# Performance work log

Hardware: AMD Instinct MI355X
Metric: run time of the kernel (lower is better)

## Reference

```python
import jax, jax.numpy as jnp
import numpy as np

B = 16384
N_DENSE = 13
N_TABLES = 26
VOCAB = 100000
DIM = 64
BOTTOM_DIMS = [13, 512, 256, 64]
TOP_DIMS = [442, 512, 256, 1]
TOP_SIGMOID_POS = 2  # sigmoid on last top layer; bottom uses relu everywhere


def _init_mlp(key, dims, scale=0.05):
    ws, bs = [], []
    for i in range(len(dims) - 1):
        key, k = jax.random.split(key)
        ws.append(jax.random.normal(k, (dims[i], dims[i + 1]), dtype=jnp.float32) * scale)
        bs.append(jnp.zeros((dims[i + 1],), dtype=jnp.float32))
    return ws, bs


def setup_inputs() -> dict:
    key = jax.random.key(0)
    k_dense, k_sparse, k_tab, k_b, k_t = jax.random.split(key, 5)
    dense_inputs = jax.random.normal(k_dense, (B, N_DENSE), dtype=jnp.float32)
    sparse_inputs = jax.random.randint(k_sparse, (B, N_TABLES), 0, VOCAB, dtype=jnp.int64)
    tables = jax.random.normal(k_tab, (N_TABLES, VOCAB, DIM), dtype=jnp.float32) * 0.01
    bws, bbs = _init_mlp(k_b, BOTTOM_DIMS)
    tws, tbs = _init_mlp(k_t, TOP_DIMS)
    return {
        'dense_inputs': dense_inputs, 'sparse_inputs': sparse_inputs, 'tables': tables,
        'bw1': bws[0], 'bb1': bbs[0], 'bw2': bws[1], 'bb2': bbs[1], 'bw3': bws[2], 'bb3': bbs[2],
        'tw1': tws[0], 'tb1': tbs[0], 'tw2': tws[1], 'tb2': tbs[1], 'tw3': tws[2], 'tb3': tbs[2],
    }


def _mlp(x, ws, bs, sigmoid_pos):
    for i, (w, b) in enumerate(zip(ws, bs)):
        x = x @ w + b
        x = jax.nn.sigmoid(x) if (sigmoid_pos is not None and i == sigmoid_pos) else jax.nn.relu(x)
    return x


def reference(dense_inputs, sparse_inputs, tables,
              bw1, bb1, bw2, bb2, bw3, bb3,
              tw1, tb1, tw2, tb2, tw3, tb3):
    # Bottom MLP: [B,13] -> [B,64], relu on every layer
    dx = _mlp(dense_inputs, [bw1, bw2, bw3], [bb1, bb2, bb3], None)
    # Multi-table embedding gather: [B,26] -> [B,26,64]
    sx = tables[jnp.arange(N_TABLES)[None, :], sparse_inputs]
    # Dot interaction (self_interaction=True): stack dense + sparse fields
    T = jnp.concatenate([dx[:, None, :], sx], axis=1)          # [B, 27, 64]
    Z = jnp.einsum('bfd,bgd->bfg', T, T)                        # [B, 27, 27]
    F = N_TABLES + 1
    iu, ju = jnp.triu_indices(F, k=0)                           # include diagonal
    flat = Z[:, iu, ju]                                         # [B, 378]
    interaction = jnp.concatenate([dx, flat], axis=1)           # [B, 442]
    # Top MLP with sigmoid on the last layer
    return _mlp(interaction, [tw1, tw2, tw3], [tb1, tb2, tb3], TOP_SIGMOID_POS)
```

## Files before the change

kernel.cpp:

```cpp
#include <hip/hip_runtime.h>

typedef unsigned short u16;
typedef _Float16 f16;
typedef __attribute__((ext_vector_type(8))) _Float16 half8;
typedef __attribute__((ext_vector_type(4))) float f32x4;
typedef __attribute__((ext_vector_type(16))) float f32x16;

#define DEV __device__ __forceinline__

static constexpr int BATCH   = 16384;
static constexpr int NTAB    = 26;
static constexpr int VOCAB   = 100000;
static constexpr int DIM     = 64;

DEV u16 f2h(float f){ union { f16 h; u16 u; } x; x.h = (f16)f; return x.u; }

DEV void llds16(u16* dst, const u16* src){
  __builtin_amdgcn_global_load_lds(
      (const __attribute__((address_space(1))) unsigned*)src,
      (__attribute__((address_space(3))) unsigned*)dst, 16, 0, 0);
}

DEV int crow(int reg, int half){ return (reg & 3) + 8 * (reg >> 2) + 4 * half; }

DEV void wtile(const float* __restrict__ src, u16* __restrict__ dst,
               int K, int N, int Kpad, int tile)
{
  __shared__ float ld[32][33];
  const int nt = N >> 5;
  const int k0 = (tile / nt) << 5;
  const int n0 = (tile % nt) << 5;
  const int tx = threadIdx.x & 31;
  const int ty = threadIdx.x >> 5;
  #pragma unroll
  for (int it = 0; it < 4; ++it) {
    int k = k0 + ty + 8 * it;
    ld[ty + 8 * it][tx] = (k < K) ? src[(size_t)k * N + n0 + tx] : 0.f;
  }
  __syncthreads();
  #pragma unroll
  for (int it = 0; it < 4; ++it) {
    int n  = n0 + ty + 8 * it;
    int kp = k0 + tx;
    dst[(size_t)n * Kpad + kp] = f2h(ld[tx][ty + 8 * it]);
  }
}

__global__ void prep_k(const float* __restrict__ dense, u16* __restrict__ Xs,
                       const float* __restrict__ bw1, u16* __restrict__ W1s,
                       const float* __restrict__ bw2, u16* __restrict__ W2s,
                       const float* __restrict__ bw3, u16* __restrict__ W3s,
                       const float* __restrict__ tw1, u16* __restrict__ WT1s,
                       const float* __restrict__ tw2, u16* __restrict__ WT2s)
{
  int blk = blockIdx.x;
  if (blk < 2048) {
    int i = blk * 256 + threadIdx.x;
    int b = i >> 5, k = i & 31;
    float v = (k < 13) ? dense[b * 13 + k] : 0.f;
    Xs[(size_t)b * 32 + k] = f2h(v);
  }
  else if (blk < 2064) wtile(bw1, W1s, 13, 512, 32,    blk - 2048);
  else if (blk < 2192) wtile(bw2, W2s, 512, 256, 512,  blk - 2064);
  else if (blk < 2208) wtile(bw3, W3s, 256, 64, 256,   blk - 2192);
  else if (blk < 2464) wtile(tw1, WT1s, 442, 512, 512, blk - 2208);
  else                 wtile(tw2, WT2s, 512, 256, 512, blk - 2464);
}

__global__ __launch_bounds__(512)
void mega_k(const u16* __restrict__ Xs, const u16* __restrict__ W1s,
            const u16* __restrict__ W2s, const u16* __restrict__ W3s,
            const float* __restrict__ bb1, const float* __restrict__ bb2,
            const float* __restrict__ bb3, const int* __restrict__ sidx,
            const float* __restrict__ tables, const u16* __restrict__ WT1s,
            const u16* __restrict__ WT2s, const float* __restrict__ tb1,
            const float* __restrict__ tb2, const float* __restrict__ tw3,
            const float* __restrict__ tb3, float* __restrict__ out)
{
  __shared__ alignas(16) u16 lds[71680];
  __shared__ float redbuf[8][64];
  u16* AB   = lds;
  u16* R1   = lds + 32768;
  u16* Xl   = R1;
  u16* W1l  = R1 + 2048;
  u16* W2b0 = R1 + 18432;
  u16* W2b1 = R1;
  u16* A2   = R1 + 18432;
  u16* W3l  = R1;
  u16* dxl  = R1 + 34816;
  u16* Wb0  = R1;
  u16* Wb1  = R1 + 16384;

  const int tid = threadIdx.x, lane = tid & 63, wid = tid >> 6;
  int bid = blockIdx.x;
  bid = (bid & 7) * 32 + (bid >> 3);
  const int m0  = bid * 64;
  const int l31 = lane & 31, half = lane >> 5;

  auto stageW2 = [&](int t, u16* buf) {
    #pragma unroll
    for (int it = 0; it < 4; ++it) {
      int loff = (it * 512 + tid) * 16;
      int row  = loff >> 7, slot = (loff & 127) >> 4, gs = slot ^ (row & 7);
      llds16(buf + (size_t)(it * 512 + (wid << 6)) * 8,
             W2s + (size_t)row * 512 + t * 64 + gs * 8);
    }
  };

  if (tid < 256) {
    int loff = tid * 16, row = loff >> 6, slot = (loff & 63) >> 4, gs = slot ^ (row & 3);
    llds16(Xl + (size_t)(wid << 6) * 8, Xs + (size_t)(m0 + row) * 32 + gs * 8);
  }
  #pragma unroll
  for (int it = 0; it < 4; ++it) {
    int loff = (it * 512 + tid) * 16, row = loff >> 6, slot = (loff & 63) >> 4,
        gs = slot ^ (row & 3);
    llds16(W1l + (size_t)(it * 512 + (wid << 6)) * 8, W1s + (size_t)row * 32 + gs * 8);
  }
  stageW2(0, W2b0);
  asm volatile("s_waitcnt vmcnt(4)" ::: "memory");
  __builtin_amdgcn_s_barrier();

  {
    f32x16 acc1[2][2] = {};
    #pragma unroll
    for (int ks = 0; ks < 2; ++ks) {
      half8 af[2], bf[2];
      #pragma unroll
      for (int mi = 0; mi < 2; ++mi) {
        int row = mi * 32 + l31, sl = (2 * ks + half) ^ (row & 3);
        af[mi] = *(const half8*)(Xl + (size_t)row * 32 + sl * 8);
      }
      #pragma unroll
      for (int ni = 0; ni < 2; ++ni) {
        int row = wid * 64 + ni * 32 + l31, sl = (2 * ks + half) ^ (row & 3);
        bf[ni] = *(const half8*)(W1l + (size_t)row * 32 + sl * 8);
      }
      #pragma unroll
      for (int mi = 0; mi < 2; ++mi)
        #pragma unroll
        for (int ni = 0; ni < 2; ++ni)
          acc1[mi][ni] = __builtin_amdgcn_mfma_f32_32x32x16_f16(af[mi], bf[ni], acc1[mi][ni], 0, 0, 0);
    }
    #pragma unroll
    for (int ni = 0; ni < 2; ++ni) {
      int col = wid * 64 + ni * 32 + l31;
      float bv = bb1[col];
      #pragma unroll
      for (int mi = 0; mi < 2; ++mi)
        #pragma unroll
        for (int reg = 0; reg < 16; ++reg) {
          int row = mi * 32 + crow(reg, half);
          float v = fmaxf(acc1[mi][ni][reg] + bv, 0.f);
          AB[(size_t)row * 512 + (((col >> 3) ^ (row & 63)) * 8) + (col & 7)] = f2h(v);
        }
    }
  }
  __syncthreads();

  {
    f32x16 acc2[2] = {};
    for (int t = 0; t < 8; ++t) {
      asm volatile("s_waitcnt vmcnt(0)" ::: "memory");
      __builtin_amdgcn_s_barrier();
      if (t < 7) stageW2(t + 1, ((t + 1) & 1) ? W2b1 : W2b0);
      const u16* buf = (t & 1) ? W2b1 : W2b0;
      #pragma unroll
      for (int ks = 0; ks < 4; ++ks) {
        int s = t * 4 + ks;
        half8 af[2], bf;
        #pragma unroll
        for (int mi = 0; mi < 2; ++mi) {
          int row = mi * 32 + l31, sl = (2 * s + half) ^ (row & 63);
          af[mi] = *(const half8*)(AB + (size_t)row * 512 + sl * 8);
        }
        {
          int row = wid * 32 + l31, sl = (2 * ks + half) ^ (row & 7);
          bf = *(const half8*)(buf + (size_t)row * 64 + sl * 8);
        }
        #pragma unroll
        for (int mi = 0; mi < 2; ++mi)
          acc2[mi] = __builtin_amdgcn_mfma_f32_32x32x16_f16(af[mi], bf, acc2[mi], 0, 0, 0);
      }
    }
    int col = wid * 32 + l31;
    float bv = bb2[col];
    #pragma unroll
    for (int mi = 0; mi < 2; ++mi)
      #pragma unroll
      for (int reg = 0; reg < 16; ++reg) {
        int row = mi * 32 + crow(reg, half);
        float v = fmaxf(acc2[mi][reg] + bv, 0.f);
        A2[(size_t)row * 256 + (((col >> 3) ^ (row & 31)) * 8) + (col & 7)] = f2h(v);
      }
  }
  __syncthreads();

  #pragma unroll
  for (int it = 0; it < 4; ++it) {
    int loff = (it * 512 + tid) * 16;
    int row = loff >> 9, slot = (loff & 511) >> 4, gs = slot ^ (row & 31);
    llds16(W3l + (size_t)(it * 512 + (wid << 6)) * 8, W3s + (size_t)row * 256 + gs * 8);
  }
  asm volatile("s_waitcnt vmcnt(0)" ::: "memory");
  __builtin_amdgcn_s_barrier();

  if (wid < 4) {
    f32x16 acc3 = {};
    const int gm = (wid >> 1) * 32, gn = (wid & 1) * 32;
    #pragma unroll
    for (int s = 0; s < 16; ++s) {
      int rowa = gm + l31, sa = (2 * s + half) ^ (rowa & 31);
      half8 a = *(const half8*)(A2 + (size_t)rowa * 256 + sa * 8);
      int rowb = gn + l31, sb = (2 * s + half) ^ (rowb & 31);
      half8 b = *(const half8*)(W3l + (size_t)rowb * 256 + sb * 8);
      acc3 = __builtin_amdgcn_mfma_f32_32x32x16_f16(a, b, acc3, 0, 0, 0);
    }
    #pragma unroll
    for (int reg = 0; reg < 16; ++reg) {
      int col = gn + l31, row = gm + crow(reg, half);
      float v = fmaxf(acc3[reg] + bb3[col], 0.f);
      dxl[(size_t)row * 64 + (((col >> 3) ^ (row & 7)) * 8) + (col & 7)] = f2h(v);
    }
  }
  __syncthreads();

  auto stageW4 = [&](int t, u16* buf) {
    #pragma unroll
    for (int it = 0; it < 4; ++it) {
      int p  = (it * 512 + tid) * 16;
      int pr = p >> 7, ps = (p & 127) >> 4;
      int un = ps ^ (pr & 7);
      int row = 2 * pr + (un >> 2), ls = un & 3;
      llds16(buf + (size_t)(it * 512 + (wid << 6)) * 8,
             WT1s + (size_t)row * 512 + t * 32 + ls * 8);
    }
  };
  stageW4(0, Wb0);

  const int r = l31;
  auto gload = [&](int sr, f32x4* buf) {
    if (r >= 1 && r <= 26) {
      int id = sidx[(size_t)(m0 + sr) * NTAB + (r - 1)];
      const float* src = tables + ((size_t)(r - 1) * VOCAB + (size_t)id) * DIM;
      #pragma unroll
      for (int ks = 0; ks < 4; ++ks) {
        const float* p = src + ks * 16 + half * 8;
        buf[2 * ks]     = *(const f32x4*)(p);
        buf[2 * ks + 1] = *(const f32x4*)(p + 4);
      }
    }
  };
  auto gram = [&](int sr, const f32x4* buf) {
    {
      u16 dv = dxl[(size_t)sr * 64 + (((lane >> 3) ^ (sr & 7)) * 8) + (lane & 7)];
      AB[(size_t)sr * 512 + (((lane >> 3) ^ (sr & 63)) * 8) + (lane & 7)] = dv;
      int c = 442 + lane;
      AB[(size_t)sr * 512 + (((c >> 3) ^ (sr & 63)) * 8) + (c & 7)] = 0;
      if (lane < 6) {
        int c2 = 506 + lane;
        AB[(size_t)sr * 512 + (((c2 >> 3) ^ (sr & 63)) * 8) + (c2 & 7)] = 0;
      }
    }
    half8 fh[4];
    #pragma unroll
    for (int ks = 0; ks < 4; ++ks) {
      half8 h = {};
      if (r == 0) {
        int sl = (2 * ks + half) ^ (sr & 7);
        h = *(const half8*)(dxl + (size_t)sr * 64 + sl * 8);
      } else if (r <= 26) {
        f32x4 a = buf[2 * ks], c = buf[2 * ks + 1];
        #pragma unroll
        for (int j = 0; j < 4; ++j) { h[j] = (f16)a[j]; h[j + 4] = (f16)c[j]; }
      }
      fh[ks] = h;
    }
    f32x16 z = {};
    #pragma unroll
    for (int ks = 0; ks < 4; ++ks)
      z = __builtin_amdgcn_mfma_f32_32x32x16_f16(fh[ks], fh[ks], z, 0, 0, 0);
    if (r < 27) {
      #pragma unroll
      for (int reg = 0; reg < 16; ++reg) {
        int rw = crow(reg, half);
        if (rw <= r) {
          int c = 64 + rw * 27 - rw * (rw - 1) / 2 + (r - rw);
          AB[(size_t)sr * 512 + (((c >> 3) ^ (sr & 63)) * 8) + (c & 7)] = f2h(z[reg]);
        }
      }
    }
  };

  {
    f32x4 bufA[8], bufB[8];
    gload(wid * 8 + 0, bufA);
    #pragma unroll
    for (int jj = 0; jj < 8; jj += 2) {
      if (jj + 1 < 8) gload(wid * 8 + jj + 1, bufB);
      gram(wid * 8 + jj, bufA);
      if (jj + 2 < 8) gload(wid * 8 + jj + 2, bufA);
      if (jj + 1 < 8) gram(wid * 8 + jj + 1, bufB);
    }
  }
  __syncthreads();

  auto stageW5 = [&](int t, u16* buf) {
    #pragma unroll
    for (int it = 0; it < 4; ++it) {
      int loff = (it * 512 + tid) * 16;
      int row = loff >> 7, slot = (loff & 127) >> 4, gs = slot ^ (row & 7);
      llds16(buf + (size_t)(it * 512 + (wid << 6)) * 8,
             WT2s + (size_t)row * 512 + t * 64 + gs * 8);
    }
  };

  {
    f32x16 acc4[2][2] = {};
    for (int t = 0; t < 16; ++t) {
      asm volatile("s_waitcnt vmcnt(0)" ::: "memory");
      __builtin_amdgcn_s_barrier();
      if (t < 15) stageW4(t + 1, ((t + 1) & 1) ? Wb1 : Wb0);
      const u16* buf = (t & 1) ? Wb1 : Wb0;
      #pragma unroll
      for (int ks = 0; ks < 2; ++ks) {
        int s = t * 2 + ks;
        half8 af[2], bf[2];
        #pragma unroll
        for (int mi = 0; mi < 2; ++mi) {
          int row = mi * 32 + l31, sl = (2 * s + half) ^ (row & 63);
          af[mi] = *(const half8*)(AB + (size_t)row * 512 + sl * 8);
        }
        #pragma unroll
        for (int ni = 0; ni < 2; ++ni) {
          int n = wid * 64 + ni * 32 + l31;
          int pr = n >> 1;
          int ps = (4 * (n & 1) + 2 * ks + half) ^ (pr & 7);
          bf[ni] = *(const half8*)(buf + (size_t)pr * 64 + ps * 8);
        }
        #pragma unroll
        for (int mi = 0; mi < 2; ++mi)
          #pragma unroll
          for (int ni = 0; ni < 2; ++ni)
            acc4[mi][ni] = __builtin_amdgcn_mfma_f32_32x32x16_f16(af[mi], bf[ni], acc4[mi][ni], 0, 0, 0);
      }
    }
    __syncthreads();
    #pragma unroll
    for (int ni = 0; ni < 2; ++ni) {
      int col = wid * 64 + ni * 32 + l31;
      float bv = tb1[col];
      #pragma unroll
      for (int mi = 0; mi < 2; ++mi)
        #pragma unroll
        for (int reg = 0; reg < 16; ++reg) {
          int row = mi * 32 + crow(reg, half);
          float v = fmaxf(acc4[mi][ni][reg] + bv, 0.f);
          AB[(size_t)row * 512 + (((col >> 3) ^ (row & 63)) * 8) + (col & 7)] = f2h(v);
        }
    }
  }
  __syncthreads();

  {
    stageW5(0, Wb0);
    f32x16 acc5[2] = {};
    for (int t = 0; t < 8; ++t) {
      asm volatile("s_waitcnt vmcnt(0)" ::: "memory");
      __builtin_amdgcn_s_barrier();
      if (t < 7) stageW5(t + 1, ((t + 1) & 1) ? Wb1 : Wb0);
      const u16* buf = (t & 1) ? Wb1 : Wb0;
      #pragma unroll
      for (int ks = 0; ks < 4; ++ks) {
        int s = t * 4 + ks;
        half8 af[2], bf;
        #pragma unroll
        for (int mi = 0; mi < 2; ++mi) {
          int row = mi * 32 + l31, sl = (2 * s + half) ^ (row & 63);
          af[mi] = *(const half8*)(AB + (size_t)row * 512 + sl * 8);
        }
        {
          int row = wid * 32 + l31, sl = (2 * ks + half) ^ (row & 7);
          bf = *(const half8*)(buf + (size_t)row * 64 + sl * 8);
        }
        #pragma unroll
        for (int mi = 0; mi < 2; ++mi)
          acc5[mi] = __builtin_amdgcn_mfma_f32_32x32x16_f16(af[mi], bf, acc5[mi], 0, 0, 0);
      }
    }
    int col = wid * 32 + l31;
    float bv = tb2[col], wv = tw3[col];
    #pragma unroll
    for (int mi = 0; mi < 2; ++mi)
      #pragma unroll
      for (int reg = 0; reg < 16; ++reg) {
        float s = fmaxf(acc5[mi][reg] + bv, 0.f) * wv;
        #pragma unroll
        for (int off = 16; off; off >>= 1) s += __shfl_xor(s, off);
        if (l31 == 0) redbuf[wid][mi * 32 + crow(reg, half)] = s;
      }
  }
  __syncthreads();
  if (tid < 64) {
    float s = tb3[0];
    #pragma unroll
    for (int w = 0; w < 8; ++w) s += redbuf[w][tid];
    out[m0 + tid] = 1.f / (1.f + expf(-s));
  }
}

extern "C" void kernel_launch(void* const* d_in, const int* in_sizes, int n_in,
                              void* d_out, int out_size, void* d_ws, size_t ws_size,
                              hipStream_t stream)
{
  const float* dense  = (const float*)d_in[0];
  const int*   sidx   = (const int*)d_in[1];
  const float* tables = (const float*)d_in[2];
  const float* bw1 = (const float*)d_in[3];  const float* bb1 = (const float*)d_in[4];
  const float* bw2 = (const float*)d_in[5];  const float* bb2 = (const float*)d_in[6];
  const float* bw3 = (const float*)d_in[7];  const float* bb3 = (const float*)d_in[8];
  const float* tw1 = (const float*)d_in[9];  const float* tb1 = (const float*)d_in[10];
  const float* tw2 = (const float*)d_in[11]; const float* tb2 = (const float*)d_in[12];
  const float* tw3 = (const float*)d_in[13]; const float* tb3 = (const float*)d_in[14];
  float* out = (float*)d_out;

  char* ws = (char*)d_ws;
  size_t off = 0;
  auto alloc = [&](size_t bytes) { size_t o = off; off += (bytes + 1023) & ~(size_t)1023; return o; };

  u16*  Xs   = (u16*)(ws + alloc((size_t)BATCH * 32 * 2));
  u16*  W1s  = (u16*)(ws + alloc((size_t)512 * 32 * 2));
  u16*  W2s  = (u16*)(ws + alloc((size_t)256 * 512 * 2));
  u16*  W3s  = (u16*)(ws + alloc((size_t)64 * 256 * 2));
  u16*  WT1s = (u16*)(ws + alloc((size_t)512 * 512 * 2));
  u16*  WT2s = (u16*)(ws + alloc((size_t)256 * 512 * 2));
  (void)ws_size; (void)n_in; (void)in_sizes; (void)out_size;

  prep_k<<<2592, 256, 0, stream>>>(dense, Xs, bw1, W1s, bw2, W2s, bw3, W3s,
                                   tw1, WT1s, tw2, WT2s);
  mega_k<<<256, 512, 0, stream>>>(Xs, W1s, W2s, W3s, bb1, bb2, bb3, sidx, tables,
                                  WT1s, WT2s, tb1, tb2, tw3, tb3, out);
}
```

Baseline: 68.84 us.

## Fuse dense-input conversion into mega kernel and prefetch embedding gathers earlier

```diff
diff --git a/kernel.cpp b/kernel.cpp
--- a/kernel.cpp
+++ b/kernel.cpp
@@ -46,29 +46,22 @@
   }
 }
 
-__global__ void prep_k(const float* __restrict__ dense, u16* __restrict__ Xs,
-                       const float* __restrict__ bw1, u16* __restrict__ W1s,
+__global__ void prep_k(const float* __restrict__ bw1, u16* __restrict__ W1s,
                        const float* __restrict__ bw2, u16* __restrict__ W2s,
                        const float* __restrict__ bw3, u16* __restrict__ W3s,
                        const float* __restrict__ tw1, u16* __restrict__ WT1s,
                        const float* __restrict__ tw2, u16* __restrict__ WT2s)
 {
   int blk = blockIdx.x;
-  if (blk < 2048) {
-    int i = blk * 256 + threadIdx.x;
-    int b = i >> 5, k = i & 31;
-    float v = (k < 13) ? dense[b * 13 + k] : 0.f;
-    Xs[(size_t)b * 32 + k] = f2h(v);
-  }
-  else if (blk < 2064) wtile(bw1, W1s, 13, 512, 32,    blk - 2048);
-  else if (blk < 2192) wtile(bw2, W2s, 512, 256, 512,  blk - 2064);
-  else if (blk < 2208) wtile(bw3, W3s, 256, 64, 256,   blk - 2192);
-  else if (blk < 2464) wtile(tw1, WT1s, 442, 512, 512, blk - 2208);
-  else                 wtile(tw2, WT2s, 512, 256, 512, blk - 2464);
+  if      (blk < 16)  wtile(bw1, W1s, 13, 512, 32,    blk);
+  else if (blk < 144) wtile(bw2, W2s, 512, 256, 512,  blk - 16);
+  else if (blk < 160) wtile(bw3, W3s, 256, 64, 256,   blk - 144);
+  else if (blk < 416) wtile(tw1, WT1s, 442, 512, 512, blk - 160);
+  else                wtile(tw2, WT2s, 512, 256, 512, blk - 416);
 }
 
 __global__ __launch_bounds__(512)
-void mega_k(const u16* __restrict__ Xs, const u16* __restrict__ W1s,
+void mega_k(const float* __restrict__ dense, const u16* __restrict__ W1s,
             const u16* __restrict__ W2s, const u16* __restrict__ W3s,
             const float* __restrict__ bb1, const float* __restrict__ bb2,
             const float* __restrict__ bb3, const int* __restrict__ sidx,
@@ -107,9 +100,12 @@
     }
   };
 
-  if (tid < 256) {
-    int loff = tid * 16, row = loff >> 6, slot = (loff & 63) >> 4, gs = slot ^ (row & 3);
-    llds16(Xl + (size_t)(wid << 6) * 8, Xs + (size_t)(m0 + row) * 32 + gs * 8);
+  #pragma unroll
+  for (int i = 0; i < 4; ++i) {
+    int idx = i * 512 + tid;
+    int row = idx >> 5, col = idx & 31;
+    float v = (col < 13) ? dense[(size_t)(m0 + row) * 13 + col] : 0.f;
+    Xl[(size_t)row * 32 + (((col >> 3) ^ (row & 3)) << 3) + (col & 7)] = f2h(v);
   }
   #pragma unroll
   for (int it = 0; it < 4; ++it) {
@@ -118,7 +114,7 @@
     llds16(W1l + (size_t)(it * 512 + (wid << 6)) * 8, W1s + (size_t)row * 32 + gs * 8);
   }
   stageW2(0, W2b0);
-  asm volatile("s_waitcnt vmcnt(4)" ::: "memory");
+  asm volatile("s_waitcnt vmcnt(4) lgkmcnt(0)" ::: "memory");
   __builtin_amdgcn_s_barrier();
 
   {
@@ -196,13 +192,38 @@
   }
   __syncthreads();
 
+  const int r = l31;
+  int myid[8];
+  #pragma unroll
+  for (int j = 0; j < 8; ++j) myid[j] = 0;
+  if (r >= 1 && r <= 26) {
+    #pragma unroll
+    for (int j = 0; j < 8; ++j)
+      myid[j] = sidx[(size_t)(m0 + wid * 8 + j) * NTAB + (r - 1)];
+  }
+
   #pragma unroll
   for (int it = 0; it < 4; ++it) {
     int loff = (it * 512 + tid) * 16;
     int row = loff >> 9, slot = (loff & 511) >> 4, gs = slot ^ (row & 31);
     llds16(W3l + (size_t)(it * 512 + (wid << 6)) * 8, W3s + (size_t)row * 256 + gs * 8);
   }
-  asm volatile("s_waitcnt vmcnt(0)" ::: "memory");
+
+  f32x4 bufA[8], bufB[8];
+  auto gload = [&](int id, f32x4* buf) {
+    if (r >= 1 && r <= 26) {
+      const float* src = tables + ((size_t)(r - 1) * VOCAB + (size_t)id) * DIM;
+      #pragma unroll
+      for (int ks = 0; ks < 4; ++ks) {
+        const float* p = src + ks * 16 + half * 8;
+        buf[2 * ks]     = *(const f32x4*)(p);
+        buf[2 * ks + 1] = *(const f32x4*)(p + 4);
+      }
+    }
+  };
+  gload(myid[0], bufA);
+  gload(myid[1], bufB);
+  asm volatile("s_waitcnt vmcnt(16)" ::: "memory");
   __builtin_amdgcn_s_barrier();
 
   if (wid < 4) {
@@ -223,7 +244,8 @@
       dxl[(size_t)row * 64 + (((col >> 3) ^ (row & 7)) * 8) + (col & 7)] = f2h(v);
     }
   }
-  __syncthreads();
+  asm volatile("s_waitcnt lgkmcnt(0)" ::: "memory");
+  __builtin_amdgcn_s_barrier();
 
   auto stageW4 = [&](int t, u16* buf) {
     #pragma unroll
@@ -238,19 +260,6 @@
   };
   stageW4(0, Wb0);
 
-  const int r = l31;
-  auto gload = [&](int sr, f32x4* buf) {
-    if (r >= 1 && r <= 26) {
-      int id = sidx[(size_t)(m0 + sr) * NTAB + (r - 1)];
-      const float* src = tables + ((size_t)(r - 1) * VOCAB + (size_t)id) * DIM;
-      #pragma unroll
-      for (int ks = 0; ks < 4; ++ks) {
-        const float* p = src + ks * 16 + half * 8;
-        buf[2 * ks]     = *(const f32x4*)(p);
-        buf[2 * ks + 1] = *(const f32x4*)(p + 4);
-      }
-    }
-  };
   auto gram = [&](int sr, const f32x4* buf) {
     {
       u16 dv = dxl[(size_t)sr * 64 + (((lane >> 3) ^ (sr & 7)) * 8) + (lane & 7)];
@@ -292,16 +301,12 @@
     }
   };
 
-  {
-    f32x4 bufA[8], bufB[8];
-    gload(wid * 8 + 0, bufA);
-    #pragma unroll
-    for (int jj = 0; jj < 8; jj += 2) {
-      if (jj + 1 < 8) gload(wid * 8 + jj + 1, bufB);
-      gram(wid * 8 + jj, bufA);
-      if (jj + 2 < 8) gload(wid * 8 + jj + 2, bufA);
-      if (jj + 1 < 8) gram(wid * 8 + jj + 1, bufB);
-    }
+  #pragma unroll
+  for (int jj = 0; jj < 8; jj += 2) {
+    gram(wid * 8 + jj, bufA);
+    if (jj + 2 < 8) gload(myid[jj + 2], bufA);
+    gram(wid * 8 + jj + 1, bufB);
+    if (jj + 3 < 8) gload(myid[jj + 3], bufB);
   }
   __syncthreads();
 
@@ -428,7 +433,6 @@
   size_t off = 0;
   auto alloc = [&](size_t bytes) { size_t o = off; off += (bytes + 1023) & ~(size_t)1023; return o; };
 
-  u16*  Xs   = (u16*)(ws + alloc((size_t)BATCH * 32 * 2));
   u16*  W1s  = (u16*)(ws + alloc((size_t)512 * 32 * 2));
   u16*  W2s  = (u16*)(ws + alloc((size_t)256 * 512 * 2));
   u16*  W3s  = (u16*)(ws + alloc((size_t)64 * 256 * 2));
@@ -436,8 +440,7 @@
   u16*  WT2s = (u16*)(ws + alloc((size_t)256 * 512 * 2));
   (void)ws_size; (void)n_in; (void)in_sizes; (void)out_size;
 
-  prep_k<<<2592, 256, 0, stream>>>(dense, Xs, bw1, W1s, bw2, W2s, bw3, W3s,
-                                   tw1, WT1s, tw2, WT2s);
-  mega_k<<<256, 512, 0, stream>>>(Xs, W1s, W2s, W3s, bb1, bb2, bb3, sidx, tables,
+  prep_k<<<544, 256, 0, stream>>>(bw1, W1s, bw2, W2s, bw3, W3s, tw1, WT1s, tw2, WT2s);
+  mega_k<<<256, 512, 0, stream>>>(dense, W1s, W2s, W3s, bb1, bb2, bb3, sidx, tables,
                                   WT1s, WT2s, tb1, tb2, tw3, tb3, out);
 }
```

After: 72.68 us. 1.06x slower.

## Halve per-block batch tile to 32 rows and launch 512 blocks

Applied to the files above, without the earlier changes.

```diff
diff --git a/kernel.cpp b/kernel.cpp
--- a/kernel.cpp
+++ b/kernel.cpp
@@ -67,7 +67,7 @@
   else                 wtile(tw2, WT2s, 512, 256, 512, blk - 2464);
 }
 
-__global__ __launch_bounds__(512)
+__global__ __launch_bounds__(512, 4)
 void mega_k(const u16* __restrict__ Xs, const u16* __restrict__ W1s,
             const u16* __restrict__ W2s, const u16* __restrict__ W3s,
             const float* __restrict__ bb1, const float* __restrict__ bb2,
@@ -77,148 +77,133 @@
             const float* __restrict__ tb2, const float* __restrict__ tw3,
             const float* __restrict__ tb3, float* __restrict__ out)
 {
-  __shared__ alignas(16) u16 lds[71680];
-  __shared__ float redbuf[8][64];
+  __shared__ alignas(16) u16 lds[35840];
+  __shared__ float redbuf[8][32];
   u16* AB   = lds;
-  u16* R1   = lds + 32768;
-  u16* Xl   = R1;
-  u16* W1l  = R1 + 2048;
-  u16* W2b0 = R1 + 18432;
-  u16* W2b1 = R1;
-  u16* A2   = R1 + 18432;
-  u16* W3l  = R1;
-  u16* dxl  = R1 + 34816;
-  u16* Wb0  = R1;
-  u16* Wb1  = R1 + 16384;
+  u16* Wreg = lds + 16384;
+  u16* Wb0  = Wreg;
+  u16* Wb1  = Wreg + 8192;
+  u16* Xl   = lds + 32768;
+  u16* dxl  = lds + 33792;
 
   const int tid = threadIdx.x, lane = tid & 63, wid = tid >> 6;
   int bid = blockIdx.x;
-  bid = (bid & 7) * 32 + (bid >> 3);
-  const int m0  = bid * 64;
+  bid = (bid & 7) * 64 + (bid >> 3);
+  const int m0  = bid * 32;
   const int l31 = lane & 31, half = lane >> 5;
 
-  auto stageW2 = [&](int t, u16* buf) {
-    #pragma unroll
-    for (int it = 0; it < 4; ++it) {
-      int loff = (it * 512 + tid) * 16;
-      int row  = loff >> 7, slot = (loff & 127) >> 4, gs = slot ^ (row & 7);
-      llds16(buf + (size_t)(it * 512 + (wid << 6)) * 8,
-             W2s + (size_t)row * 512 + t * 64 + gs * 8);
-    }
-  };
-
-  if (tid < 256) {
-    int loff = tid * 16, row = loff >> 6, slot = (loff & 63) >> 4, gs = slot ^ (row & 3);
+  if (tid < 128) {
+    int p = tid * 16, row = p >> 6, slot = (p & 63) >> 4, gs = slot ^ (row & 3);
     llds16(Xl + (size_t)(wid << 6) * 8, Xs + (size_t)(m0 + row) * 32 + gs * 8);
   }
   #pragma unroll
   for (int it = 0; it < 4; ++it) {
-    int loff = (it * 512 + tid) * 16, row = loff >> 6, slot = (loff & 63) >> 4,
+    int p = (it * 512 + tid) * 16, row = p >> 6, slot = (p & 63) >> 4,
         gs = slot ^ (row & 3);
-    llds16(W1l + (size_t)(it * 512 + (wid << 6)) * 8, W1s + (size_t)row * 32 + gs * 8);
-  }
-  stageW2(0, W2b0);
-  asm volatile("s_waitcnt vmcnt(4)" ::: "memory");
+    llds16(Wreg + (size_t)(it * 512 + (wid << 6)) * 8, W1s + (size_t)row * 32 + gs * 8);
+  }
+  asm volatile("s_waitcnt vmcnt(0)" ::: "memory");
   __builtin_amdgcn_s_barrier();
 
   {
-    f32x16 acc1[2][2] = {};
+    f32x16 acc1[2] = {};
     #pragma unroll
     for (int ks = 0; ks < 2; ++ks) {
-      half8 af[2], bf[2];
-      #pragma unroll
-      for (int mi = 0; mi < 2; ++mi) {
-        int row = mi * 32 + l31, sl = (2 * ks + half) ^ (row & 3);
-        af[mi] = *(const half8*)(Xl + (size_t)row * 32 + sl * 8);
+      half8 af, bf[2];
+      {
+        int row = l31, sl = (2 * ks + half) ^ (row & 3);
+        af = *(const half8*)(Xl + (size_t)row * 32 + sl * 8);
       }
       #pragma unroll
       for (int ni = 0; ni < 2; ++ni) {
         int row = wid * 64 + ni * 32 + l31, sl = (2 * ks + half) ^ (row & 3);
-        bf[ni] = *(const half8*)(W1l + (size_t)row * 32 + sl * 8);
-      }
-      #pragma unroll
-      for (int mi = 0; mi < 2; ++mi)
-        #pragma unroll
-        for (int ni = 0; ni < 2; ++ni)
-          acc1[mi][ni] = __builtin_amdgcn_mfma_f32_32x32x16_f16(af[mi], bf[ni], acc1[mi][ni], 0, 0, 0);
+        bf[ni] = *(const half8*)(Wreg + (size_t)row * 32 + sl * 8);
+      }
+      #pragma unroll
+      for (int ni = 0; ni < 2; ++ni)
+        acc1[ni] = __builtin_amdgcn_mfma_f32_32x32x16_f16(af, bf[ni], acc1[ni], 0, 0, 0);
     }
     #pragma unroll
     for (int ni = 0; ni < 2; ++ni) {
       int col = wid * 64 + ni * 32 + l31;
       float bv = bb1[col];
       #pragma unroll
-      for (int mi = 0; mi < 2; ++mi)
-        #pragma unroll
-        for (int reg = 0; reg < 16; ++reg) {
-          int row = mi * 32 + crow(reg, half);
-          float v = fmaxf(acc1[mi][ni][reg] + bv, 0.f);
-          AB[(size_t)row * 512 + (((col >> 3) ^ (row & 63)) * 8) + (col & 7)] = f2h(v);
-        }
-    }
-  }
-  __syncthreads();
-
+      for (int reg = 0; reg < 16; ++reg) {
+        int row = crow(reg, half);
+        float v = fmaxf(acc1[ni][reg] + bv, 0.f);
+        AB[(size_t)row * 512 + (((col >> 3) ^ (row & 31)) * 8) + (col & 7)] = f2h(v);
+      }
+    }
+  }
+  __syncthreads();
+
+  auto stageW2 = [&](int t, u16* buf) {
+    #pragma unroll
+    for (int it = 0; it < 2; ++it) {
+      int p = (it * 512 + tid) * 16, row = p >> 6, slot = (p & 63) >> 4,
+          gs = slot ^ (row & 3);
+      llds16(buf + (size_t)(it * 512 + (wid << 6)) * 8,
+             W2s + (size_t)row * 512 + t * 32 + gs * 8);
+    }
+  };
   {
-    f32x16 acc2[2] = {};
-    for (int t = 0; t < 8; ++t) {
+    stageW2(0, Wb0);
+    f32x16 acc2 = {};
+    for (int t = 0; t < 16; ++t) {
       asm volatile("s_waitcnt vmcnt(0)" ::: "memory");
       __builtin_amdgcn_s_barrier();
-      if (t < 7) stageW2(t + 1, ((t + 1) & 1) ? W2b1 : W2b0);
-      const u16* buf = (t & 1) ? W2b1 : W2b0;
-      #pragma unroll
-      for (int ks = 0; ks < 4; ++ks) {
-        int s = t * 4 + ks;
-        half8 af[2], bf;
-        #pragma unroll
-        for (int mi = 0; mi < 2; ++mi) {
-          int row = mi * 32 + l31, sl = (2 * s + half) ^ (row & 63);
-          af[mi] = *(const half8*)(AB + (size_t)row * 512 + sl * 8);
-        }
+      if (t < 15) stageW2(t + 1, ((t + 1) & 1) ? Wb1 : Wb0);
+      const u16* buf = (t & 1) ? Wb1 : Wb0;
+      #pragma unroll
+      for (int ks = 0; ks < 2; ++ks) {
+        int s = t * 2 + ks;
+        half8 af, bf;
         {
-          int row = wid * 32 + l31, sl = (2 * ks + half) ^ (row & 7);
-          bf = *(const half8*)(buf + (size_t)row * 64 + sl * 8);
-        }
-        #pragma unroll
-        for (int mi = 0; mi < 2; ++mi)
-          acc2[mi] = __builtin_amdgcn_mfma_f32_32x32x16_f16(af[mi], bf, acc2[mi], 0, 0, 0);
-      }
-    }
+          int row = l31, sl = (2 * s + half) ^ (row & 31);
+          af = *(const half8*)(AB + (size_t)row * 512 + sl * 8);
+        }
+        {
+          int row = wid * 32 + l31, sl = (2 * ks + half) ^ (row & 3);
+          bf = *(const half8*)(buf + (size_t)row * 32 + sl * 8);
+        }
+        acc2 = __builtin_amdgcn_mfma_f32_32x32x16_f16(af, bf, acc2, 0, 0, 0);
+      }
+    }
+    __syncthreads();
     int col = wid * 32 + l31;
     float bv = bb2[col];
     #pragma unroll
-    for (int mi = 0; mi < 2; ++mi)
-      #pragma unroll
-      for (int reg = 0; reg < 16; ++reg) {
-        int row = mi * 32 + crow(reg, half);
-        float v = fmaxf(acc2[mi][reg] + bv, 0.f);
-        A2[(size_t)row * 256 + (((col >> 3) ^ (row & 31)) * 8) + (col & 7)] = f2h(v);
-      }
+    for (int reg = 0; reg < 16; ++reg) {
+      int row = crow(reg, half);
+      float v = fmaxf(acc2[reg] + bv, 0.f);
+      AB[(size_t)row * 256 + (((col >> 3) ^ (row & 31)) * 8) + (col & 7)] = f2h(v);
+    }
   }
   __syncthreads();
 
   #pragma unroll
   for (int it = 0; it < 4; ++it) {
-    int loff = (it * 512 + tid) * 16;
-    int row = loff >> 9, slot = (loff & 511) >> 4, gs = slot ^ (row & 31);
-    llds16(W3l + (size_t)(it * 512 + (wid << 6)) * 8, W3s + (size_t)row * 256 + gs * 8);
+    int p = (it * 512 + tid) * 16, row = p >> 9, slot = (p & 511) >> 4,
+        gs = slot ^ (row & 31);
+    llds16(Wreg + (size_t)(it * 512 + (wid << 6)) * 8, W3s + (size_t)row * 256 + gs * 8);
   }
   asm volatile("s_waitcnt vmcnt(0)" ::: "memory");
   __builtin_amdgcn_s_barrier();
 
-  if (wid < 4) {
+  if (wid < 2) {
     f32x16 acc3 = {};
-    const int gm = (wid >> 1) * 32, gn = (wid & 1) * 32;
+    const int gn = wid * 32;
     #pragma unroll
     for (int s = 0; s < 16; ++s) {
-      int rowa = gm + l31, sa = (2 * s + half) ^ (rowa & 31);
-      half8 a = *(const half8*)(A2 + (size_t)rowa * 256 + sa * 8);
+      int rowa = l31, sa = (2 * s + half) ^ (rowa & 31);
+      half8 a = *(const half8*)(AB + (size_t)rowa * 256 + sa * 8);
       int rowb = gn + l31, sb = (2 * s + half) ^ (rowb & 31);
-      half8 b = *(const half8*)(W3l + (size_t)rowb * 256 + sb * 8);
+      half8 b = *(const half8*)(Wreg + (size_t)rowb * 256 + sb * 8);
       acc3 = __builtin_amdgcn_mfma_f32_32x32x16_f16(a, b, acc3, 0, 0, 0);
     }
     #pragma unroll
     for (int reg = 0; reg < 16; ++reg) {
-      int col = gn + l31, row = gm + crow(reg, half);
+      int col = gn + l31, row = crow(reg, half);
       float v = fmaxf(acc3[reg] + bb3[col], 0.f);
       dxl[(size_t)row * 64 + (((col >> 3) ^ (row & 7)) * 8) + (col & 7)] = f2h(v);
     }
@@ -227,181 +212,164 @@
 
   auto stageW4 = [&](int t, u16* buf) {
     #pragma unroll
-    for (int it = 0; it < 4; ++it) {
+    for (int it = 0; it < 2; ++it) {
       int p  = (it * 512 + tid) * 16;
       int pr = p >> 7, ps = (p & 127) >> 4;
       int un = ps ^ (pr & 7);
-      int row = 2 * pr + (un >> 2), ls = un & 3;
+      int n  = 4 * pr + (un >> 1), ls = un & 1;
       llds16(buf + (size_t)(it * 512 + (wid << 6)) * 8,
-             WT1s + (size_t)row * 512 + t * 32 + ls * 8);
+             WT1s + (size_t)n * 512 + t * 16 + ls * 8);
     }
   };
   stageW4(0, Wb0);
 
   const int r = l31;
-  auto gload = [&](int sr, f32x4* buf) {
+  {
+    int myid[4];
+    #pragma unroll
+    for (int j = 0; j < 4; ++j) myid[j] = 0;
     if (r >= 1 && r <= 26) {
-      int id = sidx[(size_t)(m0 + sr) * NTAB + (r - 1)];
-      const float* src = tables + ((size_t)(r - 1) * VOCAB + (size_t)id) * DIM;
+      #pragma unroll
+      for (int j = 0; j < 4; ++j)
+        myid[j] = sidx[(size_t)(m0 + wid * 4 + j) * NTAB + (r - 1)];
+    }
+    #pragma unroll
+    for (int j = 0; j < 4; ++j) {
+      int sr = wid * 4 + j;
+      f32x4 buf[8];
+      if (r >= 1 && r <= 26) {
+        const float* src = tables + ((size_t)(r - 1) * VOCAB + (size_t)myid[j]) * DIM;
+        #pragma unroll
+        for (int ks = 0; ks < 4; ++ks) {
+          const float* p = src + ks * 16 + half * 8;
+          buf[2 * ks]     = *(const f32x4*)(p);
+          buf[2 * ks + 1] = *(const f32x4*)(p + 4);
+        }
+      }
+      {
+        u16 dv = dxl[(size_t)sr * 64 + (((lane >> 3) ^ (sr & 7)) * 8) + (lane & 7)];
+        AB[(size_t)sr * 512 + (((lane >> 3) ^ (sr & 31)) * 8) + (lane & 7)] = dv;
+        int c = 442 + lane;
+        AB[(size_t)sr * 512 + (((c >> 3) ^ (sr & 31)) * 8) + (c & 7)] = 0;
+        if (lane < 6) {
+          int c2 = 506 + lane;
+          AB[(size_t)sr * 512 + (((c2 >> 3) ^ (sr & 31)) * 8) + (c2 & 7)] = 0;
+        }
+      }
+      half8 fh[4];
       #pragma unroll
       for (int ks = 0; ks < 4; ++ks) {
-        const float* p = src + ks * 16 + half * 8;
-        buf[2 * ks]     = *(const f32x4*)(p);
-        buf[2 * ks + 1] = *(const f32x4*)(p + 4);
-      }
+        half8 h = {};
+        if (r == 0) {
+          int sl = (2 * ks + half) ^ (sr & 7);
+          h = *(const half8*)(dxl + (size_t)sr * 64 + sl * 8);
+        } else if (r <= 26) {
+          f32x4 a = buf[2 * ks], c = buf[2 * ks + 1];
+          #pragma unroll
+          for (int jj = 0; jj < 4; ++jj) { h[jj] = (f16)a[jj]; h[jj + 4] = (f16)c[jj]; }
+        }
+        fh[ks] = h;
+      }
+      f32x16 z = {};
+      #pragma unroll
+      for (int ks = 0; ks < 4; ++ks)
+        z = __builtin_amdgcn_mfma_f32_32x32x16_f16(fh[ks], fh[ks], z, 0, 0, 0);
+      if (r < 27) {
+        #pragma unroll
+        for (int reg = 0; reg < 16; ++reg) {
+          int rw = crow(reg, half);
+          if (rw <= r) {
+            int c = 64 + rw * 27 - rw * (rw - 1) / 2 + (r - rw);
+            AB[(size_t)sr * 512 + (((c >> 3) ^ (sr & 31)) * 8) + (c & 7)] = f2h(z[reg]);
+          }
+        }
+      }
+    }
+  }
+  __syncthreads();
+
+  {
+    f32x16 acc4[2] = {};
+    for (int t = 0; t < 32; ++t) {
+      asm volatile("s_waitcnt vmcnt(0)" ::: "memory");
+      __builtin_amdgcn_s_barrier();
+      if (t < 31) stageW4(t + 1, ((t + 1) & 1) ? Wb1 : Wb0);
+      const u16* buf = (t & 1) ? Wb1 : Wb0;
+      half8 af, bf[2];
+      {
+        int row = l31, sl = (2 * t + half) ^ (row & 31);
+        af = *(const half8*)(AB + (size_t)row * 512 + sl * 8);
+      }
+      #pragma unroll
+      for (int ni = 0; ni < 2; ++ni) {
+        int n = wid * 64 + ni * 32 + l31;
+        int pr = n >> 2;
+        int ps = (2 * (n & 3) + half) ^ (pr & 7);
+        bf[ni] = *(const half8*)(buf + (size_t)pr * 64 + ps * 8);
+      }
+      #pragma unroll
+      for (int ni = 0; ni < 2; ++ni)
+        acc4[ni] = __builtin_amdgcn_mfma_f32_32x32x16_f16(af, bf[ni], acc4[ni], 0, 0, 0);
+    }
+    __syncthreads();
+    #pragma unroll
+    for (int ni = 0; ni < 2; ++ni) {
+      int col = wid * 64 + ni * 32 + l31;
+      float bv = tb1[col];
+      #pragma unroll
+      for (int reg = 0; reg < 16; ++reg) {
+        int row = crow(reg, half);
+        float v = fmaxf(acc4[ni][reg] + bv, 0.f);
+        AB[(size_t)row * 512 + (((col >> 3) ^ (row & 31)) * 8) + (col & 7)] = f2h(v);
+      }
+    }
+  }
+  __syncthreads();
+
+  auto stageW5 = [&](int t, u16* buf) {
+    #pragma unroll
+    for (int it = 0; it < 2; ++it) {
+      int p = (it * 512 + tid) * 16, row = p >> 6, slot = (p & 63) >> 4,
+          gs = slot ^ (row & 3);
+      llds16(buf + (size_t)(it * 512 + (wid << 6)) * 8,
+             WT2s + (size_t)row * 512 + t * 32 + gs * 8);
     }
   };
-  auto gram = [&](int sr, const f32x4* buf) {
-    {
-      u16 dv = dxl[(size_t)sr * 64 + (((lane >> 3) ^ (sr & 7)) * 8) + (lane & 7)];
-      AB[(size_t)sr * 512 + (((lane >> 3) ^ (sr & 63)) * 8) + (lane & 7)] = dv;
-      int c = 442 + lane;
-      AB[(size_t)sr * 512 + (((c >> 3) ^ (sr & 63)) * 8) + (c & 7)] = 0;
-      if (lane < 6) {
-        int c2 = 506 + lane;
-        AB[(size_t)sr * 512 + (((c2 >> 3) ^ (sr & 63)) * 8) + (c2 & 7)] = 0;
-      }
-    }
-    half8 fh[4];
-    #pragma unroll
-    for (int ks = 0; ks < 4; ++ks) {
-      half8 h = {};
-      if (r == 0) {
-        int sl = (2 * ks + half) ^ (sr & 7);
-        h = *(const half8*)(dxl + (size_t)sr * 64 + sl * 8);
-      } else if (r <= 26) {
-        f32x4 a = buf[2 * ks], c = buf[2 * ks + 1];
-        #pragma unroll
-        for (int j = 0; j < 4; ++j) { h[j] = (f16)a[j]; h[j + 4] = (f16)c[j]; }
-      }
-      fh[ks] = h;
-    }
-    f32x16 z = {};
-    #pragma unroll
-    for (int ks = 0; ks < 4; ++ks)
-      z = __builtin_amdgcn_mfma_f32_32x32x16_f16(fh[ks], fh[ks], z, 0, 0, 0);
-    if (r < 27) {
-      #pragma unroll
-      for (int reg = 0; reg < 16; ++reg) {
-        int rw = crow(reg, half);
-        if (rw <= r) {
-          int c = 64 + rw * 27 - rw * (rw - 1) / 2 + (r - rw);
-          AB[(size_t)sr * 512 + (((c >> 3) ^ (sr & 63)) * 8) + (c & 7)] = f2h(z[reg]);
-        }
-      }
-    }
-  };
-
   {
-    f32x4 bufA[8], bufB[8];
-    gload(wid * 8 + 0, bufA);
-    #pragma unroll
-    for (int jj = 0; jj < 8; jj += 2) {
-      if (jj + 1 < 8) gload(wid * 8 + jj + 1, bufB);
-      gram(wid * 8 + jj, bufA);
-      if (jj + 2 < 8) gload(wid * 8 + jj + 2, bufA);
-      if (jj + 1 < 8) gram(wid * 8 + jj + 1, bufB);
-    }
-  }
-  __syncthreads();
-
-  auto stageW5 = [&](int t, u16* buf) {
-    #pragma unroll
-    for (int it = 0; it < 4; ++it) {
-      int loff = (it * 512 + tid) * 16;
-      int row = loff >> 7, slot = (loff & 127) >> 4, gs = slot ^ (row & 7);
-      llds16(buf + (size_t)(it * 512 + (wid << 6)) * 8,
-             WT2s + (size_t)row * 512 + t * 64 + gs * 8);
-    }
-  };
-
-  {
-    f32x16 acc4[2][2] = {};
+    stageW5(0, Wb0);
+    f32x16 acc5 = {};
     for (int t = 0; t < 16; ++t) {
       asm volatile("s_waitcnt vmcnt(0)" ::: "memory");
       __builtin_amdgcn_s_barrier();
-      if (t < 15) stageW4(t + 1, ((t + 1) & 1) ? Wb1 : Wb0);
+      if (t < 15) stageW5(t + 1, ((t + 1) & 1) ? Wb1 : Wb0);
       const u16* buf = (t & 1) ? Wb1 : Wb0;
       #pragma unroll
       for (int ks = 0; ks < 2; ++ks) {
         int s = t * 2 + ks;
-        half8 af[2], bf[2];
-        #pragma unroll
-        for (int mi = 0; mi < 2; ++mi) {
-          int row = mi * 32 + l31, sl = (2 * s + half) ^ (row & 63);
-          af[mi] = *(const half8*)(AB + (size_t)row * 512 + sl * 8);
-        }
-        #pragma unroll
-        for (int ni = 0; ni < 2; ++ni) {
-          int n = wid * 64 + ni * 32 + l31;
-          int pr = n >> 1;
-          int ps = (4 * (n & 1) + 2 * ks + half) ^ (pr & 7);
-          bf[ni] = *(const half8*)(buf + (size_t)pr * 64 + ps * 8);
-        }
-        #pragma unroll
-        for (int mi = 0; mi < 2; ++mi)
-          #pragma unroll
-          for (int ni = 0; ni < 2; ++ni)
-            acc4[mi][ni] = __builtin_amdgcn_mfma_f32_32x32x16_f16(af[mi], bf[ni], acc4[mi][ni], 0, 0, 0);
-      }
-    }
-    __syncthreads();
-    #pragma unroll
-    for (int ni = 0; ni < 2; ++ni) {
-      int col = wid * 64 + ni * 32 + l31;
-      float bv = tb1[col];
-      #pragma unroll
-      for (int mi = 0; mi < 2; ++mi)
-        #pragma unroll
-        for (int reg = 0; reg < 16; ++reg) {
-          int row = mi * 32 + crow(reg, half);
-          float v = fmaxf(acc4[mi][ni][reg] + bv, 0.f);
-          AB[(size_t)row * 512 + (((col >> 3) ^ (row & 63)) * 8) + (col & 7)] = f2h(v);
-        }
-    }
-  }
-  __syncthreads();
-
-  {
-    stageW5(0, Wb0);
-    f32x16 acc5[2] = {};
-    for (int t = 0; t < 8; ++t) {
-      asm volatile("s_waitcnt vmcnt(0)" ::: "memory");
-      __builtin_amdgcn_s_barrier();
-      if (t < 7) stageW5(t + 1, ((t + 1) & 1) ? Wb1 : Wb0);
-      const u16* buf = (t & 1) ? Wb1 : Wb0;
-      #pragma unroll
-      for (int ks = 0; ks < 4; ++ks) {
-        int s = t * 4 + ks;
-        half8 af[2], bf;
-        #pragma unroll
-        for (int mi = 0; mi < 2; ++mi) {
-          int row = mi * 32 + l31, sl = (2 * s + half) ^ (row & 63);
-          af[mi] = *(const half8*)(AB + (size_t)row * 512 + sl * 8);
-        }
+        half8 af, bf;
         {
-          int row = wid * 32 + l31, sl = (2 * ks + half) ^ (row & 7);
-          bf = *(const half8*)(buf + (size_t)row * 64 + sl * 8);
-        }
-        #pragma unroll
-        for (int mi = 0; mi < 2; ++mi)
-          acc5[mi] = __builtin_amdgcn_mfma_f32_32x32x16_f16(af[mi], bf, acc5[mi], 0, 0, 0);
+          int row = l31, sl = (2 * s + half) ^ (row & 31);
+          af = *(const half8*)(AB + (size_t)row * 512 + sl * 8);
+        }
+        {
+          int row = wid * 32 + l31, sl = (2 * ks + half) ^ (row & 3);
+          bf = *(const half8*)(buf + (size_t)row * 32 + sl * 8);
+        }
+        acc5 = __builtin_amdgcn_mfma_f32_32x32x16_f16(af, bf, acc5, 0, 0, 0);
       }
     }
     int col = wid * 32 + l31;
     float bv = tb2[col], wv = tw3[col];
     #pragma unroll
-    for (int mi = 0; mi < 2; ++mi)
-      #pragma unroll
-      for (int reg = 0; reg < 16; ++reg) {
-        float s = fmaxf(acc5[mi][reg] + bv, 0.f) * wv;
-        #pragma unroll
-        for (int off = 16; off; off >>= 1) s += __shfl_xor(s, off);
-        if (l31 == 0) redbuf[wid][mi * 32 + crow(reg, half)] = s;
-      }
-  }
-  __syncthreads();
-  if (tid < 64) {
+    for (int reg = 0; reg < 16; ++reg) {
+      float s = fmaxf(acc5[reg] + bv, 0.f) * wv;
+      #pragma unroll
+      for (int off = 16; off; off >>= 1) s += __shfl_xor(s, off);
+      if (l31 == 0) redbuf[wid][crow(reg, half)] = s;
+    }
+  }
+  __syncthreads();
+  if (tid < 32) {
     float s = tb3[0];
     #pragma unroll
     for (int w = 0; w < 8; ++w) s += redbuf[w][tid];
@@ -438,6 +406,6 @@
 
   prep_k<<<2592, 256, 0, stream>>>(dense, Xs, bw1, W1s, bw2, W2s, bw3, W3s,
                                    tw1, WT1s, tw2, WT2s);
-  mega_k<<<256, 512, 0, stream>>>(Xs, W1s, W2s, W3s, bb1, bb2, bb3, sidx, tables,
+  mega_k<<<512, 512, 0, stream>>>(Xs, W1s, W2s, W3s, bb1, bb2, bb3, sidx, tables,
                                   WT1s, WT2s, tb1, tb2, tw3, tb3, out);
 }
```

Measured after the change: 100.00 us. 1.45x slower.
